# Kernel tuning notes

Measured on AMD Instinct MI355X. Metric: run time of the kernel, lower is better.

## Reference

```python
import jax, jax.numpy as jnp
import numpy as np

B, S, D, H, DH = 4, 2048, 1024, 16, 64


def setup_inputs() -> dict:
    key = jax.random.key(0)
    ks = jax.random.split(key, 12)
    inp = {
        "query": jax.random.normal(ks[0], (B, S, D), jnp.float32),
        "key": jax.random.normal(ks[1], (B, S, D), jnp.float32),
        "value": jax.random.normal(ks[2], (B, S, D), jnp.float32),
        # causal mask, broadcast over batch and heads
        "mask": jnp.tril(jnp.ones((S, S), jnp.int32))[None, None, :, :],
        "Wq": jax.random.normal(ks[3], (D, D), jnp.float32) * 0.02,
        "bq": jnp.zeros((D,), jnp.float32),
        "Wk": jax.random.normal(ks[4], (D, D), jnp.float32) * 0.02,
        "bk": jnp.zeros((D,), jnp.float32),
        "Wv": jax.random.normal(ks[5], (D, D), jnp.float32) * 0.02,
        "bv": jnp.zeros((D,), jnp.float32),
        "Wo": jax.random.normal(ks[6], (D, D), jnp.float32) * 0.02,
        "bo": jnp.zeros((D,), jnp.float32),
    }
    return inp


def reference(query, key, value, mask, Wq, bq, Wk, bk, Wv, bv, Wo, bo):
    # linear projections (torch Linear: x @ W^T + b; here W stored as [in, out])
    q = query @ Wq + bq
    k = key @ Wk + bk
    v = value @ Wv + bv
    # [B, S, D] -> [B, H, S, DH]
    q = q.reshape(B, S, H, DH).transpose(0, 2, 1, 3)
    k = k.reshape(B, S, H, DH).transpose(0, 2, 1, 3)
    v = v.reshape(B, S, H, DH).transpose(0, 2, 1, 3)
    # materialized O(S^2) attention scores
    scores = jnp.einsum("bhqd,bhkd->bhqk", q, k) * (DH ** -0.5)
    scores = jnp.where(mask == 0, jnp.float32(-jnp.inf), scores)
    attn = jax.nn.softmax(scores, axis=-1)  # dropout is identity in eval
    x = jnp.einsum("bhqk,bhkd->bhqd", attn, v)
    # [B, H, S, DH] -> [B, S, D]
    x = x.transpose(0, 2, 1, 3).reshape(B, S, D)
    out = x @ Wo + bo
    return out
```

## Files before the change

### kernel.cpp

```cpp
#include <hip/hip_runtime.h>
#include <hip/hip_bf16.h>


typedef __bf16 bf16x8 __attribute__((ext_vector_type(8)));
typedef float f32x4 __attribute__((ext_vector_type(4)));

#define GLOBAL_AS __attribute__((address_space(1)))
#define LDS_AS __attribute__((address_space(3)))

#if __has_builtin(__builtin_amdgcn_exp2f)
#define EXP2(x) __builtin_amdgcn_exp2f(x)
#else
#define EXP2(x) __expf((x) * 0.6931471805599453f)
#endif
#define QSCALE 0.18033688f

static __device__ __forceinline__ unsigned short f2bf(float f) {
    __bf16 h = (__bf16)f;
    return __builtin_bit_cast(unsigned short, h);
}

static __device__ __forceinline__ void gload_lds16(const void* g, void* l) {
    __builtin_amdgcn_global_load_lds((const GLOBAL_AS void*)g, (LDS_AS void*)l, 16, 0, 0);
}

__global__ __launch_bounds__(256) void cvt3(const float* __restrict__ q,
                                            const float* __restrict__ k,
                                            const float* __restrict__ v,
                                            unsigned short* __restrict__ dq,
                                            unsigned short* __restrict__ dk,
                                            unsigned short* __restrict__ dv, int n8) {
    const int z = blockIdx.z;
    const float* src = (z == 0) ? q : (z == 1) ? k : v;
    unsigned short* dst = (z == 0) ? dq : (z == 1) ? dk : dv;
    int i = blockIdx.x * 256 + threadIdx.x;
    if (i >= n8) return;
    const float4* s = (const float4*)src + 2 * (size_t)i;
    float4 v0 = s[0], v1 = s[1];
    unsigned short h[8] = {f2bf(v0.x), f2bf(v0.y), f2bf(v0.z), f2bf(v0.w),
                           f2bf(v1.x), f2bf(v1.y), f2bf(v1.z), f2bf(v1.w)};
    *(uint4*)(dst + 8 * (size_t)i) = *(const uint4*)h;
}

__global__ void transpose_weights(const float* __restrict__ W0, const float* __restrict__ W1,
                                  const float* __restrict__ W2, const float* __restrict__ W3,
                                  unsigned short* __restrict__ T0, unsigned short* __restrict__ T1,
                                  unsigned short* __restrict__ T2, unsigned short* __restrict__ T3) {
    const float* W; unsigned short* T;
    switch (blockIdx.z) { case 0: W=W0; T=T0; break; case 1: W=W1; T=T1; break;
                          case 2: W=W2; T=T2; break; default: W=W3; T=T3; }
    __shared__ float tile[32][33];
    int tx = threadIdx.x, ty = threadIdx.y;
    int k0 = blockIdx.x * 32, n0 = blockIdx.y * 32;
#pragma unroll
    for (int j = 0; j < 4; j++) tile[ty + 8*j][tx] = W[(size_t)(k0 + ty + 8*j) * 1024 + n0 + tx];
    __syncthreads();
#pragma unroll
    for (int j = 0; j < 4; j++) T[(size_t)(n0 + ty + 8*j) * 1024 + k0 + tx] = f2bf(tile[tx][ty + 8*j]);
}

static __device__ __forceinline__ void gemm_core(const unsigned short* __restrict__ A,
                                                 const unsigned short* __restrict__ BT,
                                                 unsigned short* Asm, unsigned short* Bsm,
                                                 int rowBase, int colBase, int t,
                                                 f32x4 acc[4][4]) {
    const int lane = t & 63, w = t >> 6;
    const int g = lane >> 4, r16 = lane & 15;
    const int wr = w >> 1, wc = w & 1;
    const int K = 1024;
    const int srow = t >> 3;
    const int scol = (t & 7) * 8;

    const unsigned short* srcA[4];
    const unsigned short* srcB[4];
#pragma unroll
    for (int j = 0; j < 4; j++) {
        srcA[j] = A  + (size_t)(rowBase + srow + 32 * j) * K + scol;
        srcB[j] = BT + (size_t)(colBase + srow + 32 * j) * K + scol;
    }
    unsigned short* dstA = Asm + 512 * w;
    unsigned short* dstB = Bsm + 512 * w;

    for (int k0 = 0; k0 < K; k0 += 64) {
        __syncthreads();
#pragma unroll
        for (int j = 0; j < 4; j++) {
            gload_lds16(srcA[j] + k0, dstA + 2048 * j);
            gload_lds16(srcB[j] + k0, dstB + 2048 * j);
        }
        __syncthreads();
#pragma unroll
        for (int ks = 0; ks < 2; ks++) {
            bf16x8 a[4], b[4];
#pragma unroll
            for (int m = 0; m < 4; m++) {
                int row = 64 * wr + 16 * m + r16;
                a[m] = *(const bf16x8*)(Asm + row * 64 + 32 * ks + 8 * g);
            }
#pragma unroll
            for (int n = 0; n < 4; n++) {
                int row = 64 * wc + 16 * n + r16;
                b[n] = *(const bf16x8*)(Bsm + row * 64 + 32 * ks + 8 * g);
            }
#pragma unroll
            for (int m = 0; m < 4; m++)
#pragma unroll
                for (int n = 0; n < 4; n++)
                    acc[m][n] = __builtin_amdgcn_mfma_f32_16x16x32_bf16(a[m], b[n], acc[m][n], 0, 0, 0);
        }
    }
}

__global__ __launch_bounds__(256) void gemm_qkv(
        const unsigned short* __restrict__ Xq, const unsigned short* __restrict__ Xk,
        const unsigned short* __restrict__ Xv,
        const unsigned short* __restrict__ WTq, const unsigned short* __restrict__ WTk,
        const unsigned short* __restrict__ WTv,
        const float* __restrict__ bq, const float* __restrict__ bk, const float* __restrict__ bv,
        unsigned short* __restrict__ Qb, unsigned short* __restrict__ Kb,
        unsigned short* __restrict__ VT) {
    __shared__ alignas(16) unsigned short Asm[8192];
    __shared__ alignas(16) unsigned short Bsm[8192];
    const int z = blockIdx.z;
    const unsigned short* A  = (z == 0) ? Xq : (z == 1) ? Xk : Xv;
    const unsigned short* BT = (z == 0) ? WTq : (z == 1) ? WTk : WTv;
    const float* bias        = (z == 0) ? bq : (z == 1) ? bk : bv;
    const int rowBase = blockIdx.y * 128, colBase = blockIdx.x * 128;
    const int t = threadIdx.x;
    const int lane = t & 63, w = t >> 6;
    const int g = lane >> 4, r16 = lane & 15;
    const int wr = w >> 1, wc = w & 1;

    f32x4 acc[4][4] = {};
    gemm_core(A, BT, Asm, Bsm, rowBase, colBase, t, acc);

    float bv4[4];
#pragma unroll
    for (int n = 0; n < 4; n++) bv4[n] = bias[colBase + 64 * wc + 16 * n + r16];

#pragma unroll
    for (int m = 0; m < 4; m++) {
#pragma unroll
        for (int n = 0; n < 4; n++) {
#pragma unroll
            for (int i = 0; i < 4; i++) {
                int row = rowBase + 64 * wr + 16 * m + 4 * g + i;
                int col = colBase + 64 * wc + 16 * n + r16;
                float v = acc[m][n][i] + bv4[n];
                int bidx = row >> 11, s = row & 2047;
                int hidx = col >> 6, dh = col & 63;
                size_t bh = (size_t)(bidx * 16 + hidx);
                if (z == 0)      Qb[(bh * 2048 + s) * 64 + dh] = f2bf(v * QSCALE);
                else if (z == 1) Kb[(bh * 2048 + s) * 64 + dh] = f2bf(v);
                else             VT[(bh * 64 + dh) * 2048 + s] = f2bf(v);
            }
        }
    }
}

__global__ __launch_bounds__(256) void gemm_out(const unsigned short* __restrict__ A,
                                                const unsigned short* __restrict__ BT,
                                                const float* __restrict__ bias,
                                                float* __restrict__ Out) {
    __shared__ alignas(16) unsigned short Asm[8192];
    __shared__ alignas(16) unsigned short Bsm[8192];
    const int rowBase = blockIdx.y * 128, colBase = blockIdx.x * 128;
    const int t = threadIdx.x;
    const int lane = t & 63, w = t >> 6;
    const int g = lane >> 4, r16 = lane & 15;
    const int wr = w >> 1, wc = w & 1;

    f32x4 acc[4][4] = {};
    gemm_core(A, BT, Asm, Bsm, rowBase, colBase, t, acc);

    float bv4[4];
#pragma unroll
    for (int n = 0; n < 4; n++) bv4[n] = bias[colBase + 64 * wc + 16 * n + r16];

#pragma unroll
    for (int m = 0; m < 4; m++)
#pragma unroll
        for (int n = 0; n < 4; n++)
#pragma unroll
            for (int i = 0; i < 4; i++) {
                int row = rowBase + 64 * wr + 16 * m + 4 * g + i;
                int col = colBase + 64 * wc + 16 * n + r16;
                Out[(size_t)row * 1024 + col] = acc[m][n][i] + bv4[n];
            }
}

static __device__ __forceinline__ void attn_step(
        const unsigned short* __restrict__ Ks, const unsigned short* __restrict__ Vs,
        const bf16x8 qfrag[2], f32x4 acco[4], float& m, float& lsum,
        int myq, int k0, bool diag,
        int g, int q16, int gh, int srcA, int srcB) {
    f32x4 accS[4] = {};
    __builtin_amdgcn_s_setprio(1);
#pragma unroll
    for (int ks = 0; ks < 2; ks++) {
#pragma unroll
        for (int tt = 0; tt < 4; tt++) {
            int row = 16 * tt + q16;
            bf16x8 ak = *(const bf16x8*)(Ks + row * 64 + ((4 * ks + g) ^ (row & 7)) * 8);
            accS[tt] = __builtin_amdgcn_mfma_f32_16x16x32_bf16(ak, qfrag[ks], accS[tt], 0, 0, 0);
        }
    }
    __builtin_amdgcn_s_setprio(0);

    float s[4][4];
#pragma unroll
    for (int tt = 0; tt < 4; tt++)
#pragma unroll
        for (int i = 0; i < 4; i++) {
            float v = accS[tt][i];
            if (diag) {
                int kg = k0 + 16 * tt + 4 * g + i;
                if (kg > myq) v = -1e30f;
            }
            s[tt][i] = v;
        }

    float pmax = s[0][0];
#pragma unroll
    for (int tt = 0; tt < 4; tt++)
#pragma unroll
        for (int i = 0; i < 4; i++) pmax = fmaxf(pmax, s[tt][i]);
    pmax = fmaxf(pmax, __shfl_xor(pmax, 16));
    pmax = fmaxf(pmax, __shfl_xor(pmax, 32));

    if (!__all(pmax <= m + 8.0f)) {
        float mnew = fmaxf(m, pmax);
        float sc = EXP2(m - mnew);
        lsum *= sc;
#pragma unroll
        for (int i = 0; i < 4; i++) {
            float sci = __shfl(sc, 4 * g + i);
#pragma unroll
            for (int d = 0; d < 4; d++) acco[d][i] *= sci;
        }
        m = mnew;
    }

    float tsum = 0.f;
    float p[4][4];
#pragma unroll
    for (int tt = 0; tt < 4; tt++)
#pragma unroll
        for (int i = 0; i < 4; i++) { p[tt][i] = EXP2(s[tt][i] - m); tsum += p[tt][i]; }
    tsum += __shfl_xor(tsum, 16);
    tsum += __shfl_xor(tsum, 32);
    lsum += tsum;

    unsigned lo[4], hi[4];
#pragma unroll
    for (int tt = 0; tt < 4; tt++) {
        lo[tt] = (unsigned)f2bf(p[tt][0]) | ((unsigned)f2bf(p[tt][1]) << 16);
        hi[tt] = (unsigned)f2bf(p[tt][2]) | ((unsigned)f2bf(p[tt][3]) << 16);
    }

#pragma unroll
    for (int ks = 0; ks < 2; ks++) {
        unsigned xa0 = __shfl(lo[2 * ks], srcA);
        unsigned xa1 = __shfl(hi[2 * ks], srcA);
        unsigned xa2 = __shfl(lo[2 * ks], srcB);
        unsigned xa3 = __shfl(hi[2 * ks], srcB);
        unsigned ya0 = __shfl(lo[2 * ks + 1], srcA);
        unsigned ya1 = __shfl(hi[2 * ks + 1], srcA);
        unsigned ya2 = __shfl(lo[2 * ks + 1], srcB);
        unsigned ya3 = __shfl(hi[2 * ks + 1], srcB);
        uint4 pw;
        pw.x = gh ? ya0 : xa0;
        pw.y = gh ? ya1 : xa1;
        pw.z = gh ? ya2 : xa2;
        pw.w = gh ? ya3 : xa3;
        bf16x8 pfrag = __builtin_bit_cast(bf16x8, pw);
        __builtin_amdgcn_s_setprio(1);
#pragma unroll
        for (int d = 0; d < 4; d++) {
            int row = 16 * d + q16;
            bf16x8 vv = *(const bf16x8*)(Vs + row * 64 + ((4 * ks + g) ^ (row & 7)) * 8);
            acco[d] = __builtin_amdgcn_mfma_f32_16x16x32_bf16(pfrag, vv, acco[d], 0, 0, 0);
        }
        __builtin_amdgcn_s_setprio(0);
    }
}

__global__ __launch_bounds__(256) void attn_kernel(const unsigned short* __restrict__ Q,
                                                   const unsigned short* __restrict__ Kb,
                                                   const unsigned short* __restrict__ VT,
                                                   unsigned short* __restrict__ Xout) {
    __shared__ alignas(16) unsigned short Ksm[2][4096];
    __shared__ alignas(16) unsigned short Vsm[2][4096];
    const int t = threadIdx.x;
    const int lane = t & 63, w = t >> 6;
    const int g = lane >> 4, q16 = lane & 15;
    const int bh = blockIdx.y;
    const int b = bh >> 4, h = bh & 15;
    const int bx = blockIdx.x;
    const int qtA = bx, qtB = 31 - bx;
    const int myqA = qtA * 64 + 16 * w + q16;
    const int myqB = qtB * 64 + 16 * w + q16;

    const int srow0 = t >> 3;
    const int ssrc = ((t & 7) ^ (srow0 & 7)) * 8;
    const unsigned short* srcK[2];
    const unsigned short* srcV[2];
#pragma unroll
    for (int j = 0; j < 2; j++) {
        int row = srow0 + 32 * j;
        srcK[j] = Kb + ((size_t)bh * 2048 + row) * 64 + ssrc;
        srcV[j] = VT + ((size_t)bh * 64 + row) * 2048 + ssrc;
    }

    const int gh = g >> 1;
    const int g0 = 2 * (g & 1);
    const int srcA = 16 * g0 + q16, srcB = srcA + 16;

    bf16x8 qfA[2], qfB[2];
    {
        const uint4* qp = (const uint4*)(Q + ((size_t)bh * 2048 + myqA) * 64);
        qfA[0] = __builtin_bit_cast(bf16x8, qp[g]);
        qfA[1] = __builtin_bit_cast(bf16x8, qp[4 + g]);
        const uint4* qq = (const uint4*)(Q + ((size_t)bh * 2048 + myqB) * 64);
        qfB[0] = __builtin_bit_cast(bf16x8, qq[g]);
        qfB[1] = __builtin_bit_cast(bf16x8, qq[4 + g]);
    }

    f32x4 accoA[4] = {}, accoB[4] = {};
    float mA = -1e30f, lsA = 0.f, mB = -1e30f, lsB = 0.f;
    int cur = 0;

#pragma unroll
    for (int j = 0; j < 2; j++) {
        gload_lds16(srcK[j], &Ksm[0][512 * w + 2048 * j]);
        gload_lds16(srcV[j], &Vsm[0][512 * w + 2048 * j]);
    }
    __syncthreads();

    const int nkt = qtB + 1;
#pragma unroll 1
    for (int kt = 0; kt < nkt; kt++) {
        if (kt + 1 < nkt) {
            int nxt = cur ^ 1;
#pragma unroll
            for (int j = 0; j < 2; j++) {
                gload_lds16(srcK[j] + (size_t)(kt + 1) * 4096, &Ksm[nxt][512 * w + 2048 * j]);
                gload_lds16(srcV[j] + (size_t)(kt + 1) * 64,   &Vsm[nxt][512 * w + 2048 * j]);
            }
        }
        const unsigned short* Ks = Ksm[cur];
        const unsigned short* Vs = Vsm[cur];
        attn_step(Ks, Vs, qfB, accoB, mB, lsB, myqB, kt * 64, kt == qtB, g, q16, gh, srcA, srcB);
        if (kt <= qtA)
            attn_step(Ks, Vs, qfA, accoA, mA, lsA, myqA, kt * 64, kt == qtA, g, q16, gh, srcA, srcB);
        __syncthreads();
        cur ^= 1;
    }

#pragma unroll
    for (int i = 0; i < 4; i++) {
        float liB = __shfl(lsB, 4 * g + i);
        float invB = 1.f / liB;
        int rowB = qtB * 64 + 16 * w + 4 * g + i;
        float liA = __shfl(lsA, 4 * g + i);
        float invA = 1.f / liA;
        int rowA = qtA * 64 + 16 * w + 4 * g + i;
#pragma unroll
        for (int d = 0; d < 4; d++) {
            int col = h * 64 + 16 * d + q16;
            Xout[((size_t)b * 2048 + rowB) * 1024 + col] = f2bf(accoB[d][i] * invB);
            Xout[((size_t)b * 2048 + rowA) * 1024 + col] = f2bf(accoA[d][i] * invA);
        }
    }
}

extern "C" void kernel_launch(void* const* d_in, const int* in_sizes, int n_in,
                              void* d_out, int out_size, void* d_ws, size_t ws_size,
                              hipStream_t stream) {
    (void)in_sizes; (void)n_in; (void)out_size; (void)ws_size;
    const float* query = (const float*)d_in[0];
    const float* key   = (const float*)d_in[1];
    const float* value = (const float*)d_in[2];
    const float* Wq = (const float*)d_in[4];
    const float* bq = (const float*)d_in[5];
    const float* Wk = (const float*)d_in[6];
    const float* bk = (const float*)d_in[7];
    const float* Wv = (const float*)d_in[8];
    const float* bv = (const float*)d_in[9];
    const float* Wo = (const float*)d_in[10];
    const float* bo = (const float*)d_in[11];

    char* base = (char*)d_ws;
    const size_t MB = 1u << 20;
    unsigned short* WTq = (unsigned short*)(base + 0 * MB);
    unsigned short* WTk = (unsigned short*)(base + 2 * MB);
    unsigned short* WTv = (unsigned short*)(base + 4 * MB);
    unsigned short* WTo = (unsigned short*)(base + 6 * MB);
    unsigned short* Qb  = (unsigned short*)(base + 8 * MB);
    unsigned short* Kbf = (unsigned short*)(base + 24 * MB);
    unsigned short* VTb = (unsigned short*)(base + 40 * MB);
    unsigned short* X   = (unsigned short*)(base + 56 * MB);

    unsigned short* Xk = (unsigned short*)d_out;
    unsigned short* Xv = Xk + (size_t)8192 * 1024;

    const int n8 = (8192 * 1024) / 8;

    transpose_weights<<<dim3(32, 32, 4), dim3(32, 8), 0, stream>>>(Wq, Wk, Wv, Wo, WTq, WTk, WTv, WTo);
    cvt3<<<dim3(4096, 1, 3), 256, 0, stream>>>(query, key, value, X, Xk, Xv, n8);
    gemm_qkv<<<dim3(8, 64, 3), 256, 0, stream>>>(X, Xk, Xv, WTq, WTk, WTv, bq, bk, bv, Qb, Kbf, VTb);
    attn_kernel<<<dim3(16, 64), 256, 0, stream>>>(Qb, Kbf, VTb, X);
    gemm_out<<<dim3(8, 64), 256, 0, stream>>>(X, WTo, bo, (float*)d_out);
}
```

Measured before the change: 408.7 us.

## Double-buffer GEMM LDS tiles and serialize paired attention query tiles

The shared GEMM core now double-buffers its A/B LDS tiles, prefetching the next K-slice while MFMAs run on the current one. This drops one barrier per iteration and doubles the GEMM kernels' LDS to 64KB. The attention kernel no longer processes its two paired query tiles together over a shared K/V stream. It runs them one after the other, each with its own K/V pass, which halves live accumulator registers but reloads K/V for the shorter tile.

```diff
diff --git a/kernel.cpp b/kernel.cpp
--- a/kernel.cpp
+++ b/kernel.cpp
@@ -81,26 +81,38 @@
     unsigned short* dstA = Asm + 512 * w;
     unsigned short* dstB = Bsm + 512 * w;
 
+#pragma unroll
+    for (int j = 0; j < 4; j++) {
+        gload_lds16(srcA[j], dstA + 2048 * j);
+        gload_lds16(srcB[j], dstB + 2048 * j);
+    }
+    __syncthreads();
+
+    int cur = 0;
     for (int k0 = 0; k0 < K; k0 += 64) {
-        __syncthreads();
-#pragma unroll
-        for (int j = 0; j < 4; j++) {
-            gload_lds16(srcA[j] + k0, dstA + 2048 * j);
-            gload_lds16(srcB[j] + k0, dstB + 2048 * j);
-        }
-        __syncthreads();
+        if (k0 + 64 < K) {
+            unsigned short* dA = dstA + (cur ^ 1) * 8192;
+            unsigned short* dB = dstB + (cur ^ 1) * 8192;
+#pragma unroll
+            for (int j = 0; j < 4; j++) {
+                gload_lds16(srcA[j] + k0 + 64, dA + 2048 * j);
+                gload_lds16(srcB[j] + k0 + 64, dB + 2048 * j);
+            }
+        }
+        const unsigned short* As = Asm + cur * 8192;
+        const unsigned short* Bs = Bsm + cur * 8192;
 #pragma unroll
         for (int ks = 0; ks < 2; ks++) {
             bf16x8 a[4], b[4];
 #pragma unroll
             for (int m = 0; m < 4; m++) {
                 int row = 64 * wr + 16 * m + r16;
-                a[m] = *(const bf16x8*)(Asm + row * 64 + 32 * ks + 8 * g);
+                a[m] = *(const bf16x8*)(As + row * 64 + 32 * ks + 8 * g);
             }
 #pragma unroll
             for (int n = 0; n < 4; n++) {
                 int row = 64 * wc + 16 * n + r16;
-                b[n] = *(const bf16x8*)(Bsm + row * 64 + 32 * ks + 8 * g);
+                b[n] = *(const bf16x8*)(Bs + row * 64 + 32 * ks + 8 * g);
             }
 #pragma unroll
             for (int m = 0; m < 4; m++)
@@ -108,6 +120,8 @@
                 for (int n = 0; n < 4; n++)
                     acc[m][n] = __builtin_amdgcn_mfma_f32_16x16x32_bf16(a[m], b[n], acc[m][n], 0, 0, 0);
         }
+        __syncthreads();
+        cur ^= 1;
     }
 }
 
@@ -119,8 +133,8 @@
         const float* __restrict__ bq, const float* __restrict__ bk, const float* __restrict__ bv,
         unsigned short* __restrict__ Qb, unsigned short* __restrict__ Kb,
         unsigned short* __restrict__ VT) {
-    __shared__ alignas(16) unsigned short Asm[8192];
-    __shared__ alignas(16) unsigned short Bsm[8192];
+    __shared__ alignas(16) unsigned short Asm[2 * 8192];
+    __shared__ alignas(16) unsigned short Bsm[2 * 8192];
     const int z = blockIdx.z;
     const unsigned short* A  = (z == 0) ? Xq : (z == 1) ? Xk : Xv;
     const unsigned short* BT = (z == 0) ? WTq : (z == 1) ? WTk : WTv;
@@ -162,8 +176,8 @@
                                                 const unsigned short* __restrict__ BT,
                                                 const float* __restrict__ bias,
                                                 float* __restrict__ Out) {
-    __shared__ alignas(16) unsigned short Asm[8192];
-    __shared__ alignas(16) unsigned short Bsm[8192];
+    __shared__ alignas(16) unsigned short Asm[2 * 8192];
+    __shared__ alignas(16) unsigned short Bsm[2 * 8192];
     const int rowBase = blockIdx.y * 128, colBase = blockIdx.x * 128;
     const int t = threadIdx.x;
     const int lane = t & 63, w = t >> 6;
@@ -296,10 +310,6 @@
     const int g = lane >> 4, q16 = lane & 15;
     const int bh = blockIdx.y;
     const int b = bh >> 4, h = bh & 15;
-    const int bx = blockIdx.x;
-    const int qtA = bx, qtB = 31 - bx;
-    const int myqA = qtA * 64 + 16 * w + q16;
-    const int myqB = qtB * 64 + 16 * w + q16;
 
     const int srow0 = t >> 3;
     const int ssrc = ((t & 7) ^ (srow0 & 7)) * 8;
@@ -316,61 +326,58 @@
     const int g0 = 2 * (g & 1);
     const int srcA = 16 * g0 + q16, srcB = srcA + 16;
 
-    bf16x8 qfA[2], qfB[2];
-    {
-        const uint4* qp = (const uint4*)(Q + ((size_t)bh * 2048 + myqA) * 64);
-        qfA[0] = __builtin_bit_cast(bf16x8, qp[g]);
-        qfA[1] = __builtin_bit_cast(bf16x8, qp[4 + g]);
-        const uint4* qq = (const uint4*)(Q + ((size_t)bh * 2048 + myqB) * 64);
-        qfB[0] = __builtin_bit_cast(bf16x8, qq[g]);
-        qfB[1] = __builtin_bit_cast(bf16x8, qq[4 + g]);
-    }
-
-    f32x4 accoA[4] = {}, accoB[4] = {};
-    float mA = -1e30f, lsA = 0.f, mB = -1e30f, lsB = 0.f;
-    int cur = 0;
-
-#pragma unroll
-    for (int j = 0; j < 2; j++) {
-        gload_lds16(srcK[j], &Ksm[0][512 * w + 2048 * j]);
-        gload_lds16(srcV[j], &Vsm[0][512 * w + 2048 * j]);
-    }
-    __syncthreads();
-
-    const int nkt = qtB + 1;
 #pragma unroll 1
-    for (int kt = 0; kt < nkt; kt++) {
-        if (kt + 1 < nkt) {
-            int nxt = cur ^ 1;
-#pragma unroll
-            for (int j = 0; j < 2; j++) {
-                gload_lds16(srcK[j] + (size_t)(kt + 1) * 4096, &Ksm[nxt][512 * w + 2048 * j]);
-                gload_lds16(srcV[j] + (size_t)(kt + 1) * 64,   &Vsm[nxt][512 * w + 2048 * j]);
-            }
-        }
-        const unsigned short* Ks = Ksm[cur];
-        const unsigned short* Vs = Vsm[cur];
-        attn_step(Ks, Vs, qfB, accoB, mB, lsB, myqB, kt * 64, kt == qtB, g, q16, gh, srcA, srcB);
-        if (kt <= qtA)
-            attn_step(Ks, Vs, qfA, accoA, mA, lsA, myqA, kt * 64, kt == qtA, g, q16, gh, srcA, srcB);
+    for (int ph = 0; ph < 2; ph++) {
+        const int qt = ph ? (31 - (int)blockIdx.x) : (int)blockIdx.x;
+        const int q0 = qt * 64;
+        const int myq = q0 + 16 * w + q16;
+        const int nkt = qt + 1;
+
+        bf16x8 qfrag[2];
+        {
+            const uint4* qp = (const uint4*)(Q + ((size_t)bh * 2048 + myq) * 64);
+            qfrag[0] = __builtin_bit_cast(bf16x8, qp[g]);
+            qfrag[1] = __builtin_bit_cast(bf16x8, qp[4 + g]);
+        }
+
+        f32x4 acco[4] = {};
+        float m = -1e30f, lsum = 0.f;
+        int cur = 0;
+
+#pragma unroll
+        for (int j = 0; j < 2; j++) {
+            gload_lds16(srcK[j], &Ksm[0][512 * w + 2048 * j]);
+            gload_lds16(srcV[j], &Vsm[0][512 * w + 2048 * j]);
+        }
         __syncthreads();
-        cur ^= 1;
-    }
-
-#pragma unroll
-    for (int i = 0; i < 4; i++) {
-        float liB = __shfl(lsB, 4 * g + i);
-        float invB = 1.f / liB;
-        int rowB = qtB * 64 + 16 * w + 4 * g + i;
-        float liA = __shfl(lsA, 4 * g + i);
-        float invA = 1.f / liA;
-        int rowA = qtA * 64 + 16 * w + 4 * g + i;
-#pragma unroll
-        for (int d = 0; d < 4; d++) {
-            int col = h * 64 + 16 * d + q16;
-            Xout[((size_t)b * 2048 + rowB) * 1024 + col] = f2bf(accoB[d][i] * invB);
-            Xout[((size_t)b * 2048 + rowA) * 1024 + col] = f2bf(accoA[d][i] * invA);
-        }
+
+        for (int kt = 0; kt < nkt; kt++) {
+            if (kt + 1 < nkt) {
+                int nxt = cur ^ 1;
+#pragma unroll
+                for (int j = 0; j < 2; j++) {
+                    gload_lds16(srcK[j] + (size_t)(kt + 1) * 4096, &Ksm[nxt][512 * w + 2048 * j]);
+                    gload_lds16(srcV[j] + (size_t)(kt + 1) * 64,   &Vsm[nxt][512 * w + 2048 * j]);
+                }
+            }
+            attn_step(Ksm[cur], Vsm[cur], qfrag, acco, m, lsum,
+                      myq, kt * 64, kt == nkt - 1, g, q16, gh, srcA, srcB);
+            __syncthreads();
+            cur ^= 1;
+        }
+
+#pragma unroll
+        for (int i = 0; i < 4; i++) {
+            float li = __shfl(lsum, 4 * g + i);
+            float inv = 1.f / li;
+            int row = q0 + 16 * w + 4 * g + i;
+#pragma unroll
+            for (int d = 0; d < 4; d++) {
+                int col = h * 64 + 16 * d + q16;
+                Xout[((size_t)b * 2048 + row) * 1024 + col] = f2bf(acco[d][i] * inv);
+            }
+        }
+        __syncthreads();
     }
 }
 
```

After: 373.7 us. -8.6%, faster.
